# Kernel tuning notes

Measured on AMD Instinct MI355X. Metric: run time of the kernel, lower is better.

## Reference

```python
import jax, jax.numpy as jnp
import numpy as np

N_NODES = 100000
N_EDGES = 3200000
IN_F = 256
OUT_F = 256


def setup_inputs() -> dict:
    key = jax.random.key(0)
    k1, k2, k3, k4, k5, k6 = jax.random.split(key, 6)
    x = jax.random.normal(k1, (N_NODES, IN_F), dtype=jnp.float32)
    edge_row = jnp.sort(jax.random.randint(k2, (N_EDGES,), 0, N_NODES, dtype=jnp.int64))
    edge_col = jax.random.randint(k3, (N_EDGES,), 0, N_NODES, dtype=jnp.int64)
    edge_val = jax.random.uniform(k4, (N_EDGES,), dtype=jnp.float32)
    stdv = 1.0 / np.sqrt(OUT_F)
    weight = jax.random.uniform(k5, (IN_F, OUT_F), dtype=jnp.float32, minval=-stdv, maxval=stdv)
    bias = jax.random.uniform(k6, (OUT_F,), dtype=jnp.float32, minval=-stdv, maxval=stdv)
    return {"x": x, "edge_row": edge_row, "edge_col": edge_col,
            "edge_val": edge_val, "weight": weight, "bias": bias}


def reference(x, edge_row, edge_col, edge_val, weight, bias):
    # support = x @ W  -> [N, out]
    support = jnp.matmul(x, weight)
    # spmm(adj, support): out[r] = sum_e val[e] * support[col[e]] for edges with row[e]==r
    gathered = support[edge_col] * edge_val[:, None]  # [E, out]
    output = jax.ops.segment_sum(gathered, edge_row, num_segments=N_NODES)
    return output + bias
```

## Files before the change

### kernel.cpp

```cpp
#include <hip/hip_runtime.h>
#include <hip/hip_bf16.h>

#define NN 100000
#define NE 3200000
#define NF 256
#define CHUNK 512

typedef __attribute__((ext_vector_type(8))) __bf16 bf16x8;
typedef __attribute__((ext_vector_type(4))) float  f32x4;


__global__ __launch_bounds__(256) void prep_w(const float* __restrict__ w,
                                              __bf16* __restrict__ wfrag,
                                              const float* __restrict__ bias,
                                              float* __restrict__ bias_p) {
    if (blockIdx.x == 32) {
        const int t = threadIdx.x;
        const int l = t >> 2, b = t & 3;
        bias_p[t] = bias[(l & 3) * 64 + 16 * b + (l >> 2)];
        return;
    }
    const int t = blockIdx.x * 256 + threadIdx.x;
    const int lane = t & 63;
    const int nf   = (t >> 6) & 15;
    const int ks   = t >> 10;
    const int col  = nf * 16 + (lane & 15);
    const int k0   = ks * 32 + (lane >> 4) * 8;
    bf16x8 v;
#pragma unroll
    for (int j = 0; j < 8; ++j) v[j] = (__bf16)w[(k0 + j) * NF + col];
    reinterpret_cast<bf16x8*>(wfrag)[t] = v;
}

__global__ __launch_bounds__(320) void gemm_q(const float* __restrict__ x,
                                              const __bf16* __restrict__ wfrag,
                                              unsigned char* __restrict__ tab,
                                              float* __restrict__ scales) {
    __shared__ __align__(16) __bf16 As[80 * 72];

    const int t    = threadIdx.x;
    const int wv   = t >> 6;
    const int lane = t & 63;
    const int row0 = blockIdx.x * 80;

    f32x4 acc[16];
#pragma unroll
    for (int nf = 0; nf < 16; ++nf) acc[nf] = (f32x4){0.f, 0.f, 0.f, 0.f};

    const int   srow = t >> 2;
    const int   sj   = (t & 3) * 8;
    const float* xp  = x + (size_t)(row0 + srow) * NF + sj;
    char* const  wr  = reinterpret_cast<char*>(As) + srow * 144 + sj * 2;

    const char* const rd =
        reinterpret_cast<const char*>(As) + (wv * 16 + (lane & 15)) * 144 + ((lane >> 4) << 4);

    const bf16x8* wf = reinterpret_cast<const bf16x8*>(wfrag);

    f32x4 s0 = __builtin_nontemporal_load(reinterpret_cast<const f32x4*>(xp));
    f32x4 s1 = __builtin_nontemporal_load(reinterpret_cast<const f32x4*>(xp + 4));

    for (int ks = 0; ks < 8; ++ks) {
        bf16x8 sb;
        sb[0] = (__bf16)s0.x; sb[1] = (__bf16)s0.y;
        sb[2] = (__bf16)s0.z; sb[3] = (__bf16)s0.w;
        sb[4] = (__bf16)s1.x; sb[5] = (__bf16)s1.y;
        sb[6] = (__bf16)s1.z; sb[7] = (__bf16)s1.w;
        *reinterpret_cast<bf16x8*>(wr) = sb;
        __syncthreads();

        if (ks < 7) {
            s0 = __builtin_nontemporal_load(
                reinterpret_cast<const f32x4*>(xp + (ks + 1) * 32));
            s1 = __builtin_nontemporal_load(
                reinterpret_cast<const f32x4*>(xp + (ks + 1) * 32 + 4));
        }

        const bf16x8 af = *reinterpret_cast<const bf16x8*>(rd);
#pragma unroll
        for (int nf = 0; nf < 16; ++nf) {
            const bf16x8 bfr = wf[(ks * 16 + nf) * 64 + lane];
            acc[nf] = __builtin_amdgcn_mfma_f32_16x16x32_bf16(af, bfr, acc[nf], 0, 0, 0);
        }
        __syncthreads();
    }

    const int hi   = lane >> 4;
    const int ccol = lane & 15;

    float m[4];
#pragma unroll
    for (int r = 0; r < 4; ++r) {
        float mm = 0.f;
#pragma unroll
        for (int nf = 0; nf < 16; ++nf) mm = fmaxf(mm, fabsf(acc[nf][r]));
        m[r] = mm;
    }
#pragma unroll
    for (int w = 1; w < 16; w <<= 1) {
#pragma unroll
        for (int r = 0; r < 4; ++r) m[r] = fmaxf(m[r], __shfl_xor(m[r], w, 64));
    }

#pragma unroll
    for (int r = 0; r < 4; ++r) {
        const int   node = row0 + wv * 16 + hi * 4 + r;
        const float isc  = 127.0f / fmaxf(m[r], 1e-30f);
        uint4 pk = {0u, 0u, 0u, 0u};
        unsigned int* pw = reinterpret_cast<unsigned int*>(&pk);
#pragma unroll
        for (int nf = 0; nf < 16; ++nf) {
            const int q = (int)rintf(acc[nf][r] * isc);
            pw[nf >> 2] |= ((unsigned int)(q & 0xff)) << ((nf & 3) * 8);
        }
        *reinterpret_cast<uint4*>(tab + (size_t)node * 256 + ccol * 16) = pk;
        if (ccol == 0) scales[node] = m[r] * (1.0f / 127.0f);
    }
}

__global__ void build_rowptr(const int* __restrict__ erow,
                             int* __restrict__ rowptr) {
    int e = blockIdx.x * blockDim.x + threadIdx.x;
    if (e >= NE) return;
    int r    = erow[e];
    int prev = (e == 0) ? -1 : erow[e - 1];
    for (int q = prev + 1; q <= r; ++q) rowptr[q] = e;
    if (e == NE - 1) {
        for (int q = r + 1; q <= NN; ++q) rowptr[q] = NE;
    }
}

__global__ __launch_bounds__(256) void spmm_f(const unsigned int* __restrict__ tab32,
                                              const int* __restrict__ rowptr,
                                              const int* __restrict__ ecol,
                                              const float* __restrict__ eval,
                                              const float* __restrict__ scales,
                                              const float* __restrict__ bias_p,
                                              float* __restrict__ out) {
    __shared__ int2 buf[CHUNK];

    const int wave = threadIdx.x >> 6;
    const int lane = threadIdx.x & 63;
    const int row  = blockIdx.x * 4 + wave;

    const int bs   = rowptr[blockIdx.x * 4];
    const int bend = rowptr[blockIdx.x * 4 + 4];
    const int rs   = rowptr[row];
    const int re   = rowptr[row + 1];

    float a0 = 0.f, a1 = 0.f, a2 = 0.f, a3 = 0.f;

    for (int cs = bs; cs < bend; cs += CHUNK) {
        const int cnt = min(CHUNK, bend - cs);
        if (cs != bs) __syncthreads();
        for (int j = threadIdx.x; j < cnt; j += 256) {
            const int   c = ecol[cs + j];
            const float v = eval[cs + j];
            buf[j] = make_int2(c, __float_as_int(v * scales[c]));
        }
        __syncthreads();

        const int lo = max(rs, cs);
        const int hi = min(re, cs + cnt);
#pragma unroll 4
        for (int i = lo; i < hi; ++i) {
            const int2  p = buf[i - cs];
            const float v = __int_as_float(p.y);
            const unsigned int g = tab32[((unsigned)p.x << 6) + lane];
            a0 = fmaf(v, (float)(int)(signed char)(g      ), a0);
            a1 = fmaf(v, (float)(int)(signed char)(g >> 8 ), a1);
            a2 = fmaf(v, (float)(int)(signed char)(g >> 16), a2);
            a3 = fmaf(v, (float)(int)(signed char)(g >> 24), a3);
        }
    }

    const f32x4 bp = *reinterpret_cast<const f32x4*>(bias_p + lane * 4);
    float* op = out + (size_t)row * NF + (lane & 3) * 64 + (lane >> 2);
    __builtin_nontemporal_store(a0 + bp.x, op);
    __builtin_nontemporal_store(a1 + bp.y, op + 16);
    __builtin_nontemporal_store(a2 + bp.z, op + 32);
    __builtin_nontemporal_store(a3 + bp.w, op + 48);
}

extern "C" void kernel_launch(void* const* d_in, const int* in_sizes, int n_in,
                              void* d_out, int out_size, void* d_ws, size_t ws_size,
                              hipStream_t stream) {
    const float* x    = (const float*)d_in[0];
    const int*   erow = (const int*)d_in[1];
    const int*   ecol = (const int*)d_in[2];
    const float* eval = (const float*)d_in[3];
    const float* w    = (const float*)d_in[4];
    const float* bias = (const float*)d_in[5];
    float*       out  = (float*)d_out;

    unsigned char* tab    = (unsigned char*)d_ws;
    int*           rowptr = (int*)((char*)d_ws + 25600000);
    __bf16*        wfrag  = (__bf16*)((char*)d_ws + 26000016);
    float*         scales = (float*)((char*)d_ws + 26131088);
    float*         bias_p = (float*)((char*)d_ws + 26531088);

    prep_w<<<33, 256, 0, stream>>>(w, wfrag, bias, bias_p);
    build_rowptr<<<(NE + 255) / 256, 256, 0, stream>>>(erow, rowptr);
    gemm_q<<<NN / 80, 320, 0, stream>>>(x, wfrag, tab, scales);
    spmm_f<<<NN / 4, 256, 0, stream>>>(
        reinterpret_cast<const unsigned int*>(tab), rowptr, ecol, eval, scales,
        bias_p, out);
}
```

Measured before the change: 196.4 us.

## Merge prep kernels, widen GEMM K-step, and use offset-unsigned int8 in SpMM

Folds the row-pointer build into the weight-prep kernel, removing one launch. The GEMM now stages 64 K-elements per barrier pair instead of 32, which halves the synchronisation count but uses more registers for the prefetch. The int8 table now stores values offset by 128 as unsigned bytes. SpMM converts them with mask-and-convert and subtracts 128 times the sum of edge weights at the end, avoiding sign-extension work per edge. The offset correction can add a small rounding error.

```diff
diff --git a/kernel.cpp b/kernel.cpp
--- a/kernel.cpp
+++ b/kernel.cpp
@@ -10,10 +10,23 @@
 typedef __attribute__((ext_vector_type(4))) float  f32x4;
 
 
-__global__ __launch_bounds__(256) void prep_w(const float* __restrict__ w,
-                                              __bf16* __restrict__ wfrag,
-                                              const float* __restrict__ bias,
-                                              float* __restrict__ bias_p) {
+__global__ __launch_bounds__(256) void prep_all(const float* __restrict__ w,
+                                                __bf16* __restrict__ wfrag,
+                                                const float* __restrict__ bias,
+                                                float* __restrict__ bias_p,
+                                                const int* __restrict__ erow,
+                                                int* __restrict__ rowptr) {
+    if (blockIdx.x >= 33) {
+        const int e = (blockIdx.x - 33) * 256 + threadIdx.x;
+        if (e >= NE) return;
+        const int r    = erow[e];
+        const int prev = (e == 0) ? -1 : erow[e - 1];
+        for (int q = prev + 1; q <= r; ++q) rowptr[q] = e;
+        if (e == NE - 1) {
+            for (int q = r + 1; q <= NN; ++q) rowptr[q] = NE;
+        }
+        return;
+    }
     if (blockIdx.x == 32) {
         const int t = threadIdx.x;
         const int l = t >> 2, b = t & 3;
@@ -47,10 +60,10 @@
 #pragma unroll
     for (int nf = 0; nf < 16; ++nf) acc[nf] = (f32x4){0.f, 0.f, 0.f, 0.f};
 
-    const int   srow = t >> 2;
-    const int   sj   = (t & 3) * 8;
-    const float* xp  = x + (size_t)(row0 + srow) * NF + sj;
-    char* const  wr  = reinterpret_cast<char*>(As) + srow * 144 + sj * 2;
+    const int    srow = t >> 2;
+    const int    sc   = (t & 3) * 16;
+    const float* xp   = x + (size_t)(row0 + srow) * NF + sc;
+    char* const  wr   = reinterpret_cast<char*>(As) + srow * 144 + sc * 2;
 
     const char* const rd =
         reinterpret_cast<const char*>(As) + (wv * 16 + (lane & 15)) * 144 + ((lane >> 4) << 4);
@@ -59,28 +72,38 @@
 
     f32x4 s0 = __builtin_nontemporal_load(reinterpret_cast<const f32x4*>(xp));
     f32x4 s1 = __builtin_nontemporal_load(reinterpret_cast<const f32x4*>(xp + 4));
-
-    for (int ks = 0; ks < 8; ++ks) {
-        bf16x8 sb;
-        sb[0] = (__bf16)s0.x; sb[1] = (__bf16)s0.y;
-        sb[2] = (__bf16)s0.z; sb[3] = (__bf16)s0.w;
-        sb[4] = (__bf16)s1.x; sb[5] = (__bf16)s1.y;
-        sb[6] = (__bf16)s1.z; sb[7] = (__bf16)s1.w;
-        *reinterpret_cast<bf16x8*>(wr) = sb;
+    f32x4 s2 = __builtin_nontemporal_load(reinterpret_cast<const f32x4*>(xp + 8));
+    f32x4 s3 = __builtin_nontemporal_load(reinterpret_cast<const f32x4*>(xp + 12));
+
+    for (int p = 0; p < 4; ++p) {
+        bf16x8 b0, b1;
+        b0[0] = (__bf16)s0.x; b0[1] = (__bf16)s0.y; b0[2] = (__bf16)s0.z; b0[3] = (__bf16)s0.w;
+        b0[4] = (__bf16)s1.x; b0[5] = (__bf16)s1.y; b0[6] = (__bf16)s1.z; b0[7] = (__bf16)s1.w;
+        b1[0] = (__bf16)s2.x; b1[1] = (__bf16)s2.y; b1[2] = (__bf16)s2.z; b1[3] = (__bf16)s2.w;
+        b1[4] = (__bf16)s3.x; b1[5] = (__bf16)s3.y; b1[6] = (__bf16)s3.z; b1[7] = (__bf16)s3.w;
+        *reinterpret_cast<bf16x8*>(wr)      = b0;
+        *reinterpret_cast<bf16x8*>(wr + 16) = b1;
         __syncthreads();
 
-        if (ks < 7) {
-            s0 = __builtin_nontemporal_load(
-                reinterpret_cast<const f32x4*>(xp + (ks + 1) * 32));
-            s1 = __builtin_nontemporal_load(
-                reinterpret_cast<const f32x4*>(xp + (ks + 1) * 32 + 4));
-        }
-
-        const bf16x8 af = *reinterpret_cast<const bf16x8*>(rd);
+        if (p < 3) {
+            const float* nx = xp + (p + 1) * 64;
+            s0 = __builtin_nontemporal_load(reinterpret_cast<const f32x4*>(nx));
+            s1 = __builtin_nontemporal_load(reinterpret_cast<const f32x4*>(nx + 4));
+            s2 = __builtin_nontemporal_load(reinterpret_cast<const f32x4*>(nx + 8));
+            s3 = __builtin_nontemporal_load(reinterpret_cast<const f32x4*>(nx + 12));
+        }
+
+        const bf16x8 af0 = *reinterpret_cast<const bf16x8*>(rd);
+        const bf16x8 af1 = *reinterpret_cast<const bf16x8*>(rd + 64);
 #pragma unroll
         for (int nf = 0; nf < 16; ++nf) {
-            const bf16x8 bfr = wf[(ks * 16 + nf) * 64 + lane];
-            acc[nf] = __builtin_amdgcn_mfma_f32_16x16x32_bf16(af, bfr, acc[nf], 0, 0, 0);
+            const bf16x8 w0 = wf[((p * 2 + 0) * 16 + nf) * 64 + lane];
+            acc[nf] = __builtin_amdgcn_mfma_f32_16x16x32_bf16(af0, w0, acc[nf], 0, 0, 0);
+        }
+#pragma unroll
+        for (int nf = 0; nf < 16; ++nf) {
+            const bf16x8 w1 = wf[((p * 2 + 1) * 16 + nf) * 64 + lane];
+            acc[nf] = __builtin_amdgcn_mfma_f32_16x16x32_bf16(af1, w1, acc[nf], 0, 0, 0);
         }
         __syncthreads();
     }
@@ -110,23 +133,11 @@
         unsigned int* pw = reinterpret_cast<unsigned int*>(&pk);
 #pragma unroll
         for (int nf = 0; nf < 16; ++nf) {
-            const int q = (int)rintf(acc[nf][r] * isc);
+            const int q = (int)rintf(acc[nf][r] * isc) + 128;
             pw[nf >> 2] |= ((unsigned int)(q & 0xff)) << ((nf & 3) * 8);
         }
         *reinterpret_cast<uint4*>(tab + (size_t)node * 256 + ccol * 16) = pk;
         if (ccol == 0) scales[node] = m[r] * (1.0f / 127.0f);
-    }
-}
-
-__global__ void build_rowptr(const int* __restrict__ erow,
-                             int* __restrict__ rowptr) {
-    int e = blockIdx.x * blockDim.x + threadIdx.x;
-    if (e >= NE) return;
-    int r    = erow[e];
-    int prev = (e == 0) ? -1 : erow[e - 1];
-    for (int q = prev + 1; q <= r; ++q) rowptr[q] = e;
-    if (e == NE - 1) {
-        for (int q = r + 1; q <= NN; ++q) rowptr[q] = NE;
     }
 }
 
@@ -148,7 +159,7 @@
     const int rs   = rowptr[row];
     const int re   = rowptr[row + 1];
 
-    float a0 = 0.f, a1 = 0.f, a2 = 0.f, a3 = 0.f;
+    float a0 = 0.f, a1 = 0.f, a2 = 0.f, a3 = 0.f, S = 0.f;
 
     for (int cs = bs; cs < bend; cs += CHUNK) {
         const int cnt = min(CHUNK, bend - cs);
@@ -167,19 +178,21 @@
             const int2  p = buf[i - cs];
             const float v = __int_as_float(p.y);
             const unsigned int g = tab32[((unsigned)p.x << 6) + lane];
-            a0 = fmaf(v, (float)(int)(signed char)(g      ), a0);
-            a1 = fmaf(v, (float)(int)(signed char)(g >> 8 ), a1);
-            a2 = fmaf(v, (float)(int)(signed char)(g >> 16), a2);
-            a3 = fmaf(v, (float)(int)(signed char)(g >> 24), a3);
+            a0 = fmaf(v, (float)(g & 0xffu), a0);
+            a1 = fmaf(v, (float)((g >> 8) & 0xffu), a1);
+            a2 = fmaf(v, (float)((g >> 16) & 0xffu), a2);
+            a3 = fmaf(v, (float)(g >> 24), a3);
+            S += v;
         }
     }
 
     const f32x4 bp = *reinterpret_cast<const f32x4*>(bias_p + lane * 4);
+    const float c128 = 128.0f * S;
     float* op = out + (size_t)row * NF + (lane & 3) * 64 + (lane >> 2);
-    __builtin_nontemporal_store(a0 + bp.x, op);
-    __builtin_nontemporal_store(a1 + bp.y, op + 16);
-    __builtin_nontemporal_store(a2 + bp.z, op + 32);
-    __builtin_nontemporal_store(a3 + bp.w, op + 48);
+    __builtin_nontemporal_store(a0 - c128 + bp.x, op);
+    __builtin_nontemporal_store(a1 - c128 + bp.y, op + 16);
+    __builtin_nontemporal_store(a2 - c128 + bp.z, op + 32);
+    __builtin_nontemporal_store(a3 - c128 + bp.w, op + 48);
 }
 
 extern "C" void kernel_launch(void* const* d_in, const int* in_sizes, int n_in,
@@ -199,8 +212,8 @@
     float*         scales = (float*)((char*)d_ws + 26131088);
     float*         bias_p = (float*)((char*)d_ws + 26531088);
 
-    prep_w<<<33, 256, 0, stream>>>(w, wfrag, bias, bias_p);
-    build_rowptr<<<(NE + 255) / 256, 256, 0, stream>>>(erow, rowptr);
+    prep_all<<<33 + (NE + 255) / 256, 256, 0, stream>>>(w, wfrag, bias, bias_p,
+                                                        erow, rowptr);
     gemm_q<<<NN / 80, 320, 0, stream>>>(x, wfrag, tab, scales);
     spmm_f<<<NN / 4, 256, 0, stream>>>(
         reinterpret_cast<const unsigned int*>(tab), rowptr, ecol, eval, scales,
```

New measurement: 196.5 us. Within noise of the previous version (+0.0%).
